# Kernel tuning notes

Measured on AMD Instinct MI355X. Metric: run time of the kernel, lower is better.

Reference implementation:

```python
import jax, jax.numpy as jnp
import numpy as np

N, E = 50000, 800000
NFEAT, NHID, HEADS, NCLASS = 256, 16, 8, 40


def _gat_conv(x, src, dst, W, att_src, att_dst, bias, heads, out_ch, concat, num_nodes):
    # x: [N, F_in]; W: [F_in, heads*out_ch]; att_*: [heads, out_ch]; bias matches output dim
    h = (x @ W).reshape(num_nodes, heads, out_ch)          # [N, H, C]
    a_src = jnp.einsum('nhc,hc->nh', h, att_src)           # [N, H]
    a_dst = jnp.einsum('nhc,hc->nh', h, att_dst)           # [N, H]
    logits = jax.nn.leaky_relu(a_src[src] + a_dst[dst], negative_slope=0.2)  # [E, H]
    # segment softmax over incoming edges of each destination node
    m = jax.ops.segment_max(logits, dst, num_segments=num_nodes)
    e = jnp.exp(logits - m[dst])
    denom = jax.ops.segment_sum(e, dst, num_segments=num_nodes)
    alpha = e / (denom[dst] + 1e-16)                       # [E, H]
    msg = h[src] * alpha[:, :, None]                       # [E, H, C]
    out = jax.ops.segment_sum(msg, dst, num_segments=num_nodes)  # [N, H, C]
    out = out.reshape(num_nodes, heads * out_ch) if concat else out.mean(axis=1)
    return out + bias


def setup_inputs() -> dict:
    key = jax.random.key(0)
    ks = jax.random.split(key, 10)
    x = jax.random.normal(ks[0], (N, NFEAT), dtype=jnp.float32)
    edge_index = jax.random.randint(ks[1], (2, E), 0, N, dtype=jnp.int64)
    s = 0.1
    W1 = jax.random.normal(ks[2], (NFEAT, HEADS * NHID), dtype=jnp.float32) * s
    att_src1 = jax.random.normal(ks[3], (HEADS, NHID), dtype=jnp.float32) * s
    att_dst1 = jax.random.normal(ks[4], (HEADS, NHID), dtype=jnp.float32) * s
    b1 = jnp.zeros((HEADS * NHID,), dtype=jnp.float32)
    W2 = jax.random.normal(ks[5], (HEADS * NHID, NCLASS), dtype=jnp.float32) * s
    att_src2 = jax.random.normal(ks[6], (1, NCLASS), dtype=jnp.float32) * s
    att_dst2 = jax.random.normal(ks[7], (1, NCLASS), dtype=jnp.float32) * s
    b2 = jnp.zeros((NCLASS,), dtype=jnp.float32)
    return dict(x=x, edge_index=edge_index, W1=W1, att_src1=att_src1, att_dst1=att_dst1,
                b1=b1, W2=W2, att_src2=att_src2, att_dst2=att_dst2, b2=b2)


def reference(x, edge_index, W1, att_src1, att_dst1, b1, W2, att_src2, att_dst2, b2):
    # add self-loops (PyG GATConv default)
    loops = jnp.arange(N, dtype=edge_index.dtype)
    src = jnp.concatenate([edge_index[0], loops])
    dst = jnp.concatenate([edge_index[1], loops])
    # dropout layers are identity in eval mode
    h = _gat_conv(x, src, dst, W1, att_src1, att_dst1, b1, HEADS, NHID, True, N)
    h = jax.nn.elu(h)
    out = _gat_conv(h, src, dst, W2, att_src2, att_dst2, b2, 1, NCLASS, False, N)
    return jax.nn.log_softmax(out, axis=1)
```

## Files before the change

### kernel.cpp

```cpp
#include <hip/hip_runtime.h>
#include <math.h>

#define NODES 50000
#define NEDGE 800000
#define ETOT  (NEDGE + NODES)
#define NF    256
#define F1    128
#define NHEAD 8
#define NHID  16
#define NC    40
#define ELLCAP 64
#define SG_BLOCKS 4103
#define SG_GEMMCUT 3910

typedef __attribute__((ext_vector_type(8))) short bf16x8;
typedef __attribute__((ext_vector_type(4))) float f32x4;
typedef __attribute__((ext_vector_type(2))) float f32x2;

__device__ __forceinline__ float bflo(unsigned u) { return __uint_as_float(u << 16); }
__device__ __forceinline__ float bfhi(unsigned u) { return __uint_as_float(u & 0xffff0000u); }
__device__ __forceinline__ unsigned short f2bf(float f) {
    unsigned u = __float_as_uint(f);
    unsigned r = u + 0x7fffu + ((u >> 16) & 1u);
    return (unsigned short)(r >> 16);
}
__device__ __forceinline__ unsigned pk2(float a, float b) {
    return (unsigned)f2bf(a) | ((unsigned)f2bf(b) << 16);
}
__device__ __forceinline__ unsigned char f2fp8(float v) {
    return (unsigned char)(__builtin_amdgcn_cvt_pk_fp8_f32(v, v, 0, false) & 0xff);
}

__global__ void detect_k(const unsigned* __restrict__ u, unsigned* __restrict__ flag) {
    int t = threadIdx.x;
    if (u[2 * t + 1] != 0u) atomicOr(flag, 1u);
}

__global__ void prepW12(const float* __restrict__ W1, const float* __restrict__ atts1,
                        const float* __restrict__ attd1,
                        const float* __restrict__ W2, const float* __restrict__ atts2,
                        const float* __restrict__ attd2,
                        unsigned short* __restrict__ W1t, unsigned short* __restrict__ W2e) {
    int b = blockIdx.x;
    int k = threadIdx.x;
    if (b < 144) {
        int n = b;
        float v;
        if (n < 128) {
            v = W1[(size_t)k * F1 + n];
        } else if (n < 136) {
            int h = n - 128; v = 0.f;
#pragma unroll
            for (int c = 0; c < 16; ++c) v += W1[(size_t)k * F1 + h * 16 + c] * atts1[h * 16 + c];
        } else {
            int h = n - 136; v = 0.f;
#pragma unroll
            for (int c = 0; c < 16; ++c) v += W1[(size_t)k * F1 + h * 16 + c] * attd1[h * 16 + c];
        }
        W1t[(size_t)n * NF + k] = f2bf(v);
    } else {
        int n = b - 144;
        if (k >= F1) return;
        float v = 0.f;
        if (n < NC) {
            v = W2[(size_t)k * NC + n];
        } else if (n == NC) {
#pragma unroll
            for (int c = 0; c < NC; ++c) v += W2[(size_t)k * NC + c] * atts2[c];
        } else if (n == NC + 1) {
#pragma unroll
            for (int c = 0; c < NC; ++c) v += W2[(size_t)k * NC + c] * attd2[c];
        }
        W2e[(size_t)n * F1 + k] = f2bf(v);
    }
}

__global__ __launch_bounds__(256) void scatter_gemm1(
        const unsigned* __restrict__ u, const unsigned* __restrict__ flag,
        int* __restrict__ fill, unsigned short* __restrict__ csr16,
        const float* __restrict__ x, const unsigned short* __restrict__ W1t,
        unsigned char* __restrict__ h1f8, float* __restrict__ as1,
        float* __restrict__ ad1) {
    __shared__ uint4 wlds[2304];
    int bid = blockIdx.x;
    int t = threadIdx.x;
    bool isGemm = (bid < SG_GEMMCUT) && ((bid % 5) == 4);
    if (!isGemm) {
        int si = bid - min(bid, SG_GEMMCUT) / 5;
        int e = si * 256 + t;
        if (e >= ETOT) return;
        int s, d;
        if (e < NEDGE) {
            if (*flag) { s = (int)u[e]; d = (int)u[NEDGE + e]; }
            else       { s = (int)u[2 * e]; d = (int)u[2 * NEDGE + 2 * e]; }
        } else s = d = e - NEDGE;
        int pos = atomicAdd(&fill[d], 1);
        if (pos < ELLCAP) csr16[((size_t)d << 6) + pos] = (unsigned short)s;
        return;
    }
    int gi = bid / 5;
    int wave = t >> 6, lane = t & 63;
    int mbase = gi * 64 + wave * 16;
    int rowc = min(mbase + (lane & 15), NODES - 1);
    int kg = lane >> 4;
    const float4* xr = (const float4*)(x + (size_t)rowc * NF + kg * 8);

    float4 xa[16];
#pragma unroll
    for (int ks = 0; ks < 8; ++ks) {
        xa[2 * ks]     = xr[ks * 8];
        xa[2 * ks + 1] = xr[ks * 8 + 1];
    }
    __builtin_amdgcn_sched_barrier(0);

    f32x4 acc[9];
#pragma unroll
    for (int f = 0; f < 9; ++f) acc[f] = (f32x4){0.f, 0.f, 0.f, 0.f};

    int r = lane & 15;
    int swz = r & 7;
    int rb = r * 16 + kg;

#pragma unroll
    for (int half = 0; half < 2; ++half) {
        if (half) __syncthreads();
#pragma unroll
        for (int it = 0; it < 9; ++it) {
            int idx = it * 256 + t;
            wlds[idx ^ ((idx >> 4) & 7)] =
                ((const uint4*)W1t)[(idx >> 4) * 32 + half * 16 + (idx & 15)];
        }
        __syncthreads();
#pragma unroll
        for (int ks = 0; ks < 4; ++ks) {
            union { uint4 u4; bf16x8 v; } A;
            float4 a0 = xa[2 * (half * 4 + ks)], a1 = xa[2 * (half * 4 + ks) + 1];
            A.u4.x = pk2(a0.x, a0.y); A.u4.y = pk2(a0.z, a0.w);
            A.u4.z = pk2(a1.x, a1.y); A.u4.w = pk2(a1.z, a1.w);
#pragma unroll
            for (int f = 0; f < 9; ++f) {
                union { uint4 u4; bf16x8 v; } B;
                B.u4 = wlds[(f * 256 + rb + ks * 4) ^ swz];
                acc[f] = __builtin_amdgcn_mfma_f32_16x16x32_bf16(A.v, B.v, acc[f], 0, 0, 0);
            }
        }
    }

    int col = lane & 15;
    int rbase = mbase + (lane >> 4) * 4;
#pragma unroll
    for (int f = 0; f < 8; ++f) {
        int wv = 0;
        wv = __builtin_amdgcn_cvt_pk_fp8_f32(acc[f][0], acc[f][1], wv, false);
        wv = __builtin_amdgcn_cvt_pk_fp8_f32(acc[f][2], acc[f][3], wv, true);
#pragma unroll
        for (int ii = 0; ii < 4; ++ii) {
            int rr = rbase + ii;
            if (rr < NODES)
                h1f8[(size_t)rr * F1 + f * 16 + col] = (unsigned char)((wv >> (8 * ii)) & 0xff);
        }
    }
#pragma unroll
    for (int ii = 0; ii < 4; ++ii) {
        int rr = rbase + ii;
        if (rr < NODES) {
            float v = acc[8][ii];
            if (col < 8) as1[(size_t)rr * NHEAD + col] = v;
            else ad1[(size_t)rr * NHEAD + (col - 8)] = v;
        }
    }
}

#define PROC8F8(AV, HV)                                          \
    {                                                            \
        float l = (AV) + adv;                                    \
        l = l > 0.f ? l : 0.2f * l;                              \
        float p = __expf(l);                                     \
        den += p;                                                \
        f32x2 c0 = __builtin_amdgcn_cvt_pk_f32_fp8(HV.x, false); \
        f32x2 c1 = __builtin_amdgcn_cvt_pk_f32_fp8(HV.x, true);  \
        f32x2 c2 = __builtin_amdgcn_cvt_pk_f32_fp8(HV.y, false); \
        f32x2 c3 = __builtin_amdgcn_cvt_pk_f32_fp8(HV.y, true);  \
        acc[0] += p * c0.x; acc[1] += p * c0.y;                  \
        acc[2] += p * c1.x; acc[3] += p * c1.y;                  \
        acc[4] += p * c2.x; acc[5] += p * c2.y;                  \
        acc[6] += p * c3.x; acc[7] += p * c3.y;                  \
    }

__global__ __launch_bounds__(256) void msg1g2(const int* __restrict__ fill,
                                              const unsigned short* __restrict__ csr16,
                                              const float* __restrict__ as1,
                                              const float* __restrict__ ad1,
                                              const unsigned char* __restrict__ h1f8,
                                              const float* __restrict__ b1,
                                              const unsigned short* __restrict__ W2e,
                                              unsigned char* __restrict__ h2f8,
                                              float* __restrict__ as2,
                                              float* __restrict__ ad2) {
    __shared__ uint4 w2s[768];
    __shared__ uint4 o1s[256];
    int t = threadIdx.x;
    int wid = t >> 6, lane = t & 63;
    int g = lane >> 4;
    int cl = lane & 15;
    int h = cl >> 1;

#pragma unroll
    for (int it = 0; it < 3; ++it) {
        int i = it * 256 + t;
        w2s[i ^ ((i >> 4) & 7)] = ((const uint4*)W2e)[i];
    }

    int d = blockIdx.x * 16 + wid * 4 + g;
    float adv = ad1[(size_t)d * NHEAD + h];
    int deg = fill[d];
    size_t eb = (size_t)d << 6;
    float den = 0.f;
    float acc[8];
#pragma unroll
    for (int k = 0; k < 8; ++k) acc[k] = 0.f;

    const char* as1c = (const char*)as1;
    unsigned hoff = (unsigned)(h << 2);
    unsigned coff = (unsigned)(cl << 3);

#define LD1(J, AV, HV)                                                \
    {                                                                 \
        int j_ = (J);                                                 \
        AV = -1e30f; HV = make_uint2(0u, 0u);                         \
        if (j_ < deg) {                                               \
            unsigned ss = (unsigned)csr16[eb + j_];                   \
            AV = *(const float*)(as1c + (ss << 5) + hoff);            \
            HV = *(const uint2*)(h1f8 + (ss << 7) + coff);            \
        }                                                             \
    }

    float av0, av1; uint2 hv0, hv1;
    LD1(0, av0, hv0);
    LD1(1, av1, hv1);
    for (int j = 0; j < deg; j += 2) {
        float ta, tb; uint2 ua, ub;
        LD1(j + 2, ta, ua);
        LD1(j + 3, tb, ub);
        PROC8F8(av0, hv0);
        PROC8F8(av1, hv1);
        av0 = ta; hv0 = ua; av1 = tb; hv1 = ub;
    }
#undef LD1

    float invd = 1.f / (den + 1e-16f);
    const float4* bp = (const float4*)(b1 + cl * 8);
    float4 ba = bp[0], bb = bp[1];
    float v[8];
    v[0] = acc[0] * invd + ba.x; v[1] = acc[1] * invd + ba.y;
    v[2] = acc[2] * invd + ba.z; v[3] = acc[3] * invd + ba.w;
    v[4] = acc[4] * invd + bb.x; v[5] = acc[5] * invd + bb.y;
    v[6] = acc[6] * invd + bb.z; v[7] = acc[7] * invd + bb.w;
#pragma unroll
    for (int k = 0; k < 8; ++k) {
        float ev = __expf(v[k]) - 1.f;
        v[k] = v[k] > 0.f ? v[k] : ev;
    }
    uint4 o;
    o.x = pk2(v[0], v[1]); o.y = pk2(v[2], v[3]);
    o.z = pk2(v[4], v[5]); o.w = pk2(v[6], v[7]);
    int orow = wid * 4 + g;
    o1s[(orow * 16 + cl) ^ (orow & 7)] = o;
    __syncthreads();

    if (wid < 3) {
        int r = lane & 15;
        int kg = lane >> 4;
        int swz = r & 7;
        f32x4 c2 = (f32x4){0.f, 0.f, 0.f, 0.f};
#pragma unroll
        for (int ks = 0; ks < 4; ++ks) {
            union { uint4 u; bf16x8 vv; } A, B;
            A.u = o1s[(r * 16 + kg + ks * 4) ^ swz];
            B.u = w2s[(wid * 256 + r * 16 + kg + ks * 4) ^ swz];
            c2 = __builtin_amdgcn_mfma_f32_16x16x32_bf16(A.vv, B.vv, c2, 0, 0, 0);
        }
        int col = lane & 15;
        int rbase = blockIdx.x * 16 + (lane >> 4) * 4;
        if (wid < 2) {
#pragma unroll
            for (int i = 0; i < 4; ++i)
                h2f8[(size_t)(rbase + i) * NC + wid * 16 + col] = f2fp8(c2[i]);
        } else {
            int c = 32 + col;
#pragma unroll
            for (int i = 0; i < 4; ++i) {
                int rr = rbase + i;
                if (c < NC) h2f8[(size_t)rr * NC + c] = f2fp8(c2[i]);
                else if (c == NC) as2[rr] = c2[i];
                else if (c == NC + 1) ad2[rr] = c2[i];
            }
        }
    }
}

__global__ __launch_bounds__(256) void msg2(const int* __restrict__ fill,
                                            const unsigned short* __restrict__ csr16,
                                            const float* __restrict__ as2,
                                            const float* __restrict__ ad2,
                                            const unsigned char* __restrict__ h2f8,
                                            const float* __restrict__ b2,
                                            float* __restrict__ out) {
    int t = threadIdx.x;
    int wid = t >> 6, lane = t & 63;
    int g = lane >> 3;
    int cl = lane & 7;
    int clc = cl < 5 ? cl : 4;
    bool act = cl < 5;
    int d0 = blockIdx.x * 32 + wid * 8 + g;
    int d = min(d0, NODES - 1);
    float adv = ad2[d];
    int deg = act ? fill[d] : 0;
    size_t eb = (size_t)d << 6;
    float den = 0.f;
    float acc[8];
#pragma unroll
    for (int k = 0; k < 8; ++k) acc[k] = 0.f;

    const char* as2c = (const char*)as2;
    unsigned coff = (unsigned)(clc << 3);

#define LD2(J, AV, HV)                                                \
    {                                                                 \
        int j_ = (J);                                                 \
        AV = -1e30f; HV = make_uint2(0u, 0u);                         \
        if (j_ < deg) {                                               \
            unsigned ss = (unsigned)csr16[eb + j_];                   \
            AV = *(const float*)(as2c + (ss << 2));                   \
            HV = *(const uint2*)(h2f8 + ss * 40u + coff);             \
        }                                                             \
    }

    float av0, av1; uint2 hv0, hv1;
    LD2(0, av0, hv0);
    LD2(1, av1, hv1);
    for (int j = 0; j < deg; j += 2) {
        float ta, tb; uint2 ua, ub;
        LD2(j + 2, ta, ua);
        LD2(j + 3, tb, ub);
        PROC8F8(av0, hv0);
        PROC8F8(av1, hv1);
        av0 = ta; hv0 = ua; av1 = tb; hv1 = ub;
    }
#undef LD2

    float invd = 1.f / (den + 1e-16f);
    float v[8];
    float mk = -1e30f;
    if (act) {
        const float4* bp = (const float4*)(b2 + cl * 8);
        float4 ba = bp[0], bb = bp[1];
        v[0] = acc[0] * invd + ba.x; v[1] = acc[1] * invd + ba.y;
        v[2] = acc[2] * invd + ba.z; v[3] = acc[3] * invd + ba.w;
        v[4] = acc[4] * invd + bb.x; v[5] = acc[5] * invd + bb.y;
        v[6] = acc[6] * invd + bb.z; v[7] = acc[7] * invd + bb.w;
#pragma unroll
        for (int k = 0; k < 8; ++k) mk = fmaxf(mk, v[k]);
    }
    mk = fmaxf(mk, __shfl_xor(mk, 1, 64));
    mk = fmaxf(mk, __shfl_xor(mk, 2, 64));
    mk = fmaxf(mk, __shfl_xor(mk, 4, 64));
    float e = 0.f;
    if (act) {
#pragma unroll
        for (int k = 0; k < 8; ++k) e += __expf(v[k] - mk);
    }
    e += __shfl_xor(e, 1, 64);
    e += __shfl_xor(e, 2, 64);
    e += __shfl_xor(e, 4, 64);
    float lse = mk + logf(e);
    if (act && d0 < NODES) {
        float4 o0 = make_float4(v[0] - lse, v[1] - lse, v[2] - lse, v[3] - lse);
        float4 o1 = make_float4(v[4] - lse, v[5] - lse, v[6] - lse, v[7] - lse);
        float* po = out + (size_t)d0 * NC + cl * 8;
        *(float4*)po = o0;
        *(float4*)(po + 4) = o1;
    }
}

extern "C" void kernel_launch(void* const* d_in, const int* in_sizes, int n_in,
                              void* d_out, int out_size, void* d_ws, size_t ws_size,
                              hipStream_t stream) {
    const float* x       = (const float*)d_in[0];
    const unsigned* eidx = (const unsigned*)d_in[1];
    const float* W1      = (const float*)d_in[2];
    const float* atts1   = (const float*)d_in[3];
    const float* attd1   = (const float*)d_in[4];
    const float* b1      = (const float*)d_in[5];
    const float* W2      = (const float*)d_in[6];
    const float* atts2   = (const float*)d_in[7];
    const float* attd2   = (const float*)d_in[8];
    const float* b2      = (const float*)d_in[9];
    float* out = (float*)d_out;

    char* base = (char*)d_ws;
    size_t off = 0;
    auto takeB = [&](size_t bytes) {
        void* p = base + off;
        off = (off + bytes + 255) & ~(size_t)255;
        return p;
    };
    unsigned* flag = (unsigned*)takeB(256);
    int* fill      = (int*)takeB((size_t)NODES * 4);
    unsigned short* csr16 = (unsigned short*)takeB((size_t)NODES * ELLCAP * 2 + 256);
    unsigned short* W1t  = (unsigned short*)takeB((size_t)144 * NF * 2);
    unsigned short* W2e  = (unsigned short*)takeB((size_t)48 * F1 * 2);
    unsigned char* h1f8  = (unsigned char*)takeB((size_t)NODES * F1);
    float* as1     = (float*)takeB((size_t)NODES * NHEAD * 4);
    float* ad1     = (float*)takeB((size_t)NODES * NHEAD * 4);
    unsigned char* h2f8  = (unsigned char*)takeB((size_t)NODES * NC + 256);
    float* as2     = (float*)takeB((size_t)NODES * 4);
    float* ad2     = (float*)takeB((size_t)NODES * 4);

    hipMemsetAsync(flag, 0, 4, stream);
    hipMemsetAsync(fill, 0, (size_t)NODES * 4, stream);

    detect_k<<<1, 256, 0, stream>>>(eidx, flag);

    prepW12<<<192, 256, 0, stream>>>(W1, atts1, attd1, W2, atts2, attd2, W1t, W2e);

    scatter_gemm1<<<SG_BLOCKS, 256, 0, stream>>>(eidx, flag, fill, csr16,
                                                 x, W1t, h1f8, as1, ad1);

    msg1g2<<<NODES / 16, 256, 0, stream>>>(fill, csr16, as1, ad1, h1f8, b1,
                                           W2e, h2f8, as2, ad2);

    msg2<<<(NODES + 31) / 32, 256, 0, stream>>>(fill, csr16, as2, ad2, h2f8, b2, out);
}
```

Before: 120.4 us.

## Inline index-width detection and quarter-size W1 LDS staging in scatter_gemm1

Removes the separate detect kernel and flag memset by having each scatter wave read the first 64 high words of the edge index and ballot to decide whether indices are int32 or int64. The GEMM part now stages W1 in four quarter-K chunks of 18 KB instead of two 36 KB halves, with a new XOR swizzle, so the shared-memory footprint of every block is halved. This is meant to raise occupancy for the many scatter blocks and cut launch overhead. The cost is two extra barrier rounds per GEMM block and a redundant 64-word load in every scatter wave.

Measured after the change: 114.6 us, median of 2. -4.8%, faster.

```diff
diff --git a/kernel.cpp b/kernel.cpp
--- a/kernel.cpp
+++ b/kernel.cpp
@@ -29,11 +29,6 @@
 }
 __device__ __forceinline__ unsigned char f2fp8(float v) {
     return (unsigned char)(__builtin_amdgcn_cvt_pk_fp8_f32(v, v, 0, false) & 0xff);
-}
-
-__global__ void detect_k(const unsigned* __restrict__ u, unsigned* __restrict__ flag) {
-    int t = threadIdx.x;
-    if (u[2 * t + 1] != 0u) atomicOr(flag, 1u);
 }
 
 __global__ void prepW12(const float* __restrict__ W1, const float* __restrict__ atts1,
@@ -76,22 +71,24 @@
 }
 
 __global__ __launch_bounds__(256) void scatter_gemm1(
-        const unsigned* __restrict__ u, const unsigned* __restrict__ flag,
+        const unsigned* __restrict__ u,
         int* __restrict__ fill, unsigned short* __restrict__ csr16,
         const float* __restrict__ x, const unsigned short* __restrict__ W1t,
         unsigned char* __restrict__ h1f8, float* __restrict__ as1,
         float* __restrict__ ad1) {
-    __shared__ uint4 wlds[2304];
+    __shared__ uint4 wlds[1152];
     int bid = blockIdx.x;
     int t = threadIdx.x;
     bool isGemm = (bid < SG_GEMMCUT) && ((bid % 5) == 4);
     if (!isGemm) {
+        unsigned hw = u[2 * (t & 63) + 1];
+        bool isi32 = __ballot(hw != 0) != 0;
         int si = bid - min(bid, SG_GEMMCUT) / 5;
         int e = si * 256 + t;
         if (e >= ETOT) return;
         int s, d;
         if (e < NEDGE) {
-            if (*flag) { s = (int)u[e]; d = (int)u[NEDGE + e]; }
+            if (isi32) { s = (int)u[e]; d = (int)u[NEDGE + e]; }
             else       { s = (int)u[2 * e]; d = (int)u[2 * NEDGE + 2 * e]; }
         } else s = d = e - NEDGE;
         int pos = atomicAdd(&fill[d], 1);
@@ -118,29 +115,31 @@
     for (int f = 0; f < 9; ++f) acc[f] = (f32x4){0.f, 0.f, 0.f, 0.f};
 
     int r = lane & 15;
-    int swz = r & 7;
-    int rb = r * 16 + kg;
-
-#pragma unroll
-    for (int half = 0; half < 2; ++half) {
-        if (half) __syncthreads();
-#pragma unroll
-        for (int it = 0; it < 9; ++it) {
-            int idx = it * 256 + t;
-            wlds[idx ^ ((idx >> 4) & 7)] =
-                ((const uint4*)W1t)[(idx >> 4) * 32 + half * 16 + (idx & 15)];
+    int rsw = r & 7;
+
+#pragma unroll
+    for (int q = 0; q < 4; ++q) {
+        if (q) __syncthreads();
+#pragma unroll
+        for (int it = 0; it < 5; ++it) {
+            int i = it * 256 + t;
+            if (i < 1152) {
+                int row = i >> 3, s = i & 7;
+                wlds[row * 8 + (s ^ (row & 7))] = ((const uint4*)W1t)[row * 32 + q * 8 + s];
+            }
         }
         __syncthreads();
 #pragma unroll
-        for (int ks = 0; ks < 4; ++ks) {
+        for (int ks2 = 0; ks2 < 2; ++ks2) {
+            int ks = q * 2 + ks2;
             union { uint4 u4; bf16x8 v; } A;
-            float4 a0 = xa[2 * (half * 4 + ks)], a1 = xa[2 * (half * 4 + ks) + 1];
+            float4 a0 = xa[2 * ks], a1 = xa[2 * ks + 1];
             A.u4.x = pk2(a0.x, a0.y); A.u4.y = pk2(a0.z, a0.w);
             A.u4.z = pk2(a1.x, a1.y); A.u4.w = pk2(a1.z, a1.w);
 #pragma unroll
             for (int f = 0; f < 9; ++f) {
                 union { uint4 u4; bf16x8 v; } B;
-                B.u4 = wlds[(f * 256 + rb + ks * 4) ^ swz];
+                B.u4 = wlds[f * 128 + r * 8 + ((ks2 * 4 + kg) ^ rsw)];
                 acc[f] = __builtin_amdgcn_mfma_f32_16x16x32_bf16(A.v, B.v, acc[f], 0, 0, 0);
             }
         }
@@ -405,7 +404,6 @@
         off = (off + bytes + 255) & ~(size_t)255;
         return p;
     };
-    unsigned* flag = (unsigned*)takeB(256);
     int* fill      = (int*)takeB((size_t)NODES * 4);
     unsigned short* csr16 = (unsigned short*)takeB((size_t)NODES * ELLCAP * 2 + 256);
     unsigned short* W1t  = (unsigned short*)takeB((size_t)144 * NF * 2);
@@ -417,14 +415,11 @@
     float* as2     = (float*)takeB((size_t)NODES * 4);
     float* ad2     = (float*)takeB((size_t)NODES * 4);
 
-    hipMemsetAsync(flag, 0, 4, stream);
     hipMemsetAsync(fill, 0, (size_t)NODES * 4, stream);
 
-    detect_k<<<1, 256, 0, stream>>>(eidx, flag);
-
     prepW12<<<192, 256, 0, stream>>>(W1, atts1, attd1, W2, atts2, attd2, W1t, W2e);
 
-    scatter_gemm1<<<SG_BLOCKS, 256, 0, stream>>>(eidx, flag, fill, csr16,
+    scatter_gemm1<<<SG_BLOCKS, 256, 0, stream>>>(eidx, fill, csr16,
                                                  x, W1t, h1f8, as1, ad1);
 
     msg1g2<<<NODES / 16, 256, 0, stream>>>(fill, csr16, as1, ad1, h1f8, b1,
```
